# Optimization experiments

Hardware: AMD Instinct MI355X
Metric: run time of the kernel (lower is better)

## Reference

```python
import jax, jax.numpy as jnp
import numpy as np

N = 8192
E = 262144
F_IN, H1, H2 = 512, 256, 128


def setup_inputs() -> dict:
    key = jax.random.key(0)
    ks = jax.random.split(key, 7)
    x = jax.random.normal(ks[0], (N, F_IN), dtype=jnp.float32)
    # glorot-ish init scale
    W1 = jax.random.normal(ks[1], (F_IN, H1), dtype=jnp.float32) * (1.0 / np.sqrt(F_IN))
    W2 = jax.random.normal(ks[2], (H1, H2), dtype=jnp.float32) * (1.0 / np.sqrt(H1))
    W3 = jax.random.normal(ks[3], (H1, H2), dtype=jnp.float32) * (1.0 / np.sqrt(H1))
    edge_w = jax.random.uniform(ks[4], (E,), dtype=jnp.float32) / 32.0  # ~normalized adj
    row = jax.random.randint(ks[5], (E,), 0, N, dtype=jnp.int64)
    col = jax.random.randint(ks[6], (E,), 0, N, dtype=jnp.int64)
    return {"x": x, "W1": W1, "W2": W2, "W3": W3, "edge_w": edge_w, "row": row, "col": col}


def _spmm(row, col, edge_w, h):
    # sparse adjacency aggregate: out[i] = sum_{e: row[e]==i} edge_w[e] * h[col[e]]
    msgs = edge_w[:, None] * h[col]  # [E, d]
    return jax.ops.segment_sum(msgs, row, num_segments=N)


def reference(x, W1, W2, W3, edge_w, row, col):
    # gc1: dropout(off, eval) -> matmul -> spmm -> relu
    h1 = jax.nn.relu(_spmm(row, col, edge_w, x @ W1))  # [N, H1]
    # gc2 / gc3: identity activation
    mu = _spmm(row, col, edge_w, h1 @ W2)              # [N, H2]
    logvar = _spmm(row, col, edge_w, h1 @ W3)          # [N, H2]
    z = mu  # eval-mode reparameterize returns mu
    adj_rec = z @ z.T  # [N, N], decoder act = identity
    return (h1, adj_rec, mu, logvar, z)
```

## Files before the change

kernel.cpp:

```cpp
#include <hip/hip_runtime.h>

typedef __bf16 bf16_t;
typedef __bf16 bf16x4 __attribute__((ext_vector_type(4)));
typedef __bf16 bf16x8 __attribute__((ext_vector_type(8)));
typedef float floatx4 __attribute__((ext_vector_type(4)));

static constexpr int NN  = 8192;
static constexpr int FIN = 512;
static constexpr int NH1 = 256;
static constexpr int NH2 = 128;
static constexpr int NE  = 262144;
static constexpr int CAP = 128;

static constexpr size_t OFF_H1     = 0;
static constexpr size_t OFF_ADJ    = (size_t)NN * NH1;
static constexpr size_t OFF_MU     = OFF_ADJ + (size_t)NN * NN;
static constexpr size_t OFF_LOGVAR = OFF_MU + (size_t)NN * NH2;
static constexpr size_t OFF_Z      = OFF_LOGVAR + (size_t)NN * NH2;

template <int KD, int RT, bool ABF, int EPI>
__device__ __forceinline__ void gemm_body(
    int bx, int by, const float* __restrict__ Af, const bf16_t* __restrict__ Abf,
    const bf16_t* __restrict__ BT, float* __restrict__ C, int ldc,
    float* __restrict__ dout, bf16_t* __restrict__ zb, int ldz,
    float* __restrict__ L, int lane, int wid) {
  const int l15 = lane & 15;
  const int lg  = lane >> 4;
  const int brow = by * (RT * 32) + (wid >> 1) * (RT * 16);
  const int bcol = bx * 128 + (wid & 1) * 64;

  floatx4 acc[RT][4];
#pragma unroll
  for (int i = 0; i < RT; ++i)
#pragma unroll
    for (int j = 0; j < 4; ++j) acc[i][j] = (floatx4){0.f, 0.f, 0.f, 0.f};

#pragma unroll 1
  for (int kk = 0; kk < KD; kk += 32) {
    bf16x8 a[RT], b[4];
#pragma unroll
    for (int rt = 0; rt < RT; ++rt) {
      const int r = brow + rt * 16 + l15;
      if constexpr (ABF) {
        a[rt] = *(const bf16x8*)(Abf + (size_t)r * KD + kk + lg * 8);
      } else {
        const float* p = Af + (size_t)r * KD + kk + lg * 8;
        const floatx4 lo = *(const floatx4*)p;
        const floatx4 hi = *(const floatx4*)(p + 4);
        bf16x8 t;
        t[0] = (bf16_t)lo[0]; t[1] = (bf16_t)lo[1];
        t[2] = (bf16_t)lo[2]; t[3] = (bf16_t)lo[3];
        t[4] = (bf16_t)hi[0]; t[5] = (bf16_t)hi[1];
        t[6] = (bf16_t)hi[2]; t[7] = (bf16_t)hi[3];
        a[rt] = t;
      }
    }
#pragma unroll
    for (int ct = 0; ct < 4; ++ct) {
      const int c = bcol + ct * 16 + l15;
      b[ct] = *(const bf16x8*)(BT + (size_t)c * KD + kk + lg * 8);
    }
#pragma unroll
    for (int rt = 0; rt < RT; ++rt)
#pragma unroll
      for (int ct = 0; ct < 4; ++ct)
        acc[rt][ct] = __builtin_amdgcn_mfma_f32_16x16x32_bf16(
            a[rt], b[ct], acc[rt][ct], 0, 0, 0);
  }

#pragma unroll
  for (int rt = 0; rt < RT; ++rt) {
#pragma unroll
    for (int ct = 0; ct < 4; ++ct)
#pragma unroll
      for (int r = 0; r < 4; ++r)
        L[(lg * 4 + r) * 68 + ct * 16 + l15] = acc[rt][ct][r];
    __builtin_amdgcn_wave_barrier();
#pragma unroll
    for (int it = 0; it < 4; ++it) {
      const int idx = it * 64 + lane;
      const int rr = idx >> 4, c4 = idx & 15;
      const floatx4 v = *(const floatx4*)(L + rr * 68 + c4 * 4);
      const int orow = brow + rt * 16 + rr;
      const int gc = bcol + c4 * 4;
      if constexpr (EPI == 0) {
        __builtin_nontemporal_store(v, (floatx4*)(C + (size_t)orow * ldc + gc));
      } else if constexpr (EPI == 1) {
        if (gc < NH2) {
          __builtin_nontemporal_store(
              v, (floatx4*)(dout + OFF_MU + (size_t)orow * NH2 + gc));
          __builtin_nontemporal_store(
              v, (floatx4*)(dout + OFF_Z + (size_t)orow * NH2 + gc));
          bf16x4 o;
          o[0] = (bf16_t)v[0]; o[1] = (bf16_t)v[1];
          o[2] = (bf16_t)v[2]; o[3] = (bf16_t)v[3];
          *(bf16x4*)(zb + (size_t)orow * ldz + gc) = o;
        } else {
          __builtin_nontemporal_store(
              v, (floatx4*)(dout + OFF_LOGVAR + (size_t)orow * NH2 + gc - NH2));
        }
      } else {
        bf16x4 o;
        o[0] = (bf16_t)v[0]; o[1] = (bf16_t)v[1];
        o[2] = (bf16_t)v[2]; o[3] = (bf16_t)v[3];
        *(bf16x4*)(zb + (size_t)orow * ldz + gc) = o;
      }
    }
    __builtin_amdgcn_wave_barrier();
  }
}

__global__ __launch_bounds__(256) void k_prep(
    const float* __restrict__ W1, const float* __restrict__ W2,
    const float* __restrict__ W3, bf16_t* __restrict__ W1T,
    bf16_t* __restrict__ W23T, int* __restrict__ counts) {
  const int gid = blockIdx.x * 256 + threadIdx.x;
  if (gid <= NN) counts[gid] = 0;
  if (gid < NH1 * FIN) {
    const int n = gid >> 9, k = gid & 511;
    W1T[gid] = (bf16_t)W1[k * NH1 + n];
  }
  if (gid < NH1 * NH1) {
    const int n = gid >> 8, k = gid & 255;
    W23T[gid] = (bf16_t)(n < NH2 ? W2[k * NH2 + n] : W3[k * NH2 + (n - NH2)]);
  }
}

__global__ __launch_bounds__(256) void k_fat(
    const float* __restrict__ x, const bf16_t* __restrict__ W1T,
    bf16_t* __restrict__ XWb, const int* __restrict__ row,
    const int* __restrict__ col, const float* __restrict__ edge_w,
    int* __restrict__ counts, uint2* __restrict__ bucket,
    uint4* __restrict__ spill) {
  __shared__ float lt[4][16 * 68];
  const int bid = blockIdx.x;
  if (bid < 256) {
    const int lane = threadIdx.x & 63;
    const int wid  = threadIdx.x >> 6;
    gemm_body<FIN, 2, false, 2>(bid & 1, bid >> 1, x, nullptr, W1T, nullptr, 0,
                                nullptr, XWb, NH1, lt[wid], lane, wid);
  } else {
    const int e = (bid - 256) * 256 + threadIdx.x;
    const int r = row[e];
    const int p = atomicAdd(&counts[r], 1);
    if (p < CAP) {
      uint2 v;
      v.x = (unsigned)col[e];
      v.y = __float_as_uint(edge_w[e]);
      bucket[(size_t)r * CAP + p] = v;
    } else {
      const int s = atomicAdd(&counts[NN], 1);
      uint4 v;
      v.x = (unsigned)r; v.y = (unsigned)col[e];
      v.z = __float_as_uint(edge_w[e]); v.w = 0;
      spill[s] = v;
    }
  }
}

template <bool RELU>
__global__ __launch_bounds__(256) void spmm_bucket(
    const int* __restrict__ counts, const uint2* __restrict__ bucket,
    const uint4* __restrict__ spill, const bf16_t* __restrict__ src,
    float* __restrict__ dst_f, bf16_t* __restrict__ dst_b) {
  const int lane = threadIdx.x & 63;
  const int r = blockIdx.x * 4 + (threadIdx.x >> 6);
  const int li = lane & 15;
  const int g  = lane >> 4;
  const int deg = min(counts[r], CAP);
  float acc[16];
#pragma unroll
  for (int c = 0; c < 16; ++c) acc[c] = 0.f;

  for (int base = 0; base < deg; base += 64) {
    const int t = base + lane;
    uint2 cw;
    cw.x = 0; cw.y = 0;
    if (t < deg) cw = bucket[(size_t)r * CAP + t];
    const int cnt = min(64, deg - base);
#pragma unroll 2
    for (int j4 = 0; j4 < cnt; j4 += 4) {
      const int cj = __shfl((int)cw.x, j4 + g);
      const float wj = __shfl(__uint_as_float(cw.y), j4 + g);
      const bf16_t* p = src + (size_t)cj * NH1 + li * 16;
      const bf16x8 v0 = *(const bf16x8*)p;
      const bf16x8 v1 = *(const bf16x8*)(p + 8);
#pragma unroll
      for (int c = 0; c < 8; ++c) {
        acc[c]     += wj * (float)v0[c];
        acc[8 + c] += wj * (float)v1[c];
      }
    }
  }
  const int ns = counts[NN];
  if (ns > 0 && g == 0) {
    for (int i = 0; i < ns; ++i) {
      const uint4 s = spill[i];
      if ((int)s.x == r) {
        const float wj = __uint_as_float(s.z);
        const bf16_t* p = src + (size_t)s.y * NH1 + li * 16;
        const bf16x8 v0 = *(const bf16x8*)p;
        const bf16x8 v1 = *(const bf16x8*)(p + 8);
#pragma unroll
        for (int c = 0; c < 8; ++c) {
          acc[c]     += wj * (float)v0[c];
          acc[8 + c] += wj * (float)v1[c];
        }
      }
    }
  }
#pragma unroll
  for (int c = 0; c < 16; ++c) {
    acc[c] += __shfl_xor(acc[c], 16);
    acc[c] += __shfl_xor(acc[c], 32);
    if constexpr (RELU) acc[c] = fmaxf(acc[c], 0.f);
  }
  float o0, o1, o2, o3;
  switch (g) {
    case 0:  o0 = acc[0];  o1 = acc[1];  o2 = acc[2];  o3 = acc[3];  break;
    case 1:  o0 = acc[4];  o1 = acc[5];  o2 = acc[6];  o3 = acc[7];  break;
    case 2:  o0 = acc[8];  o1 = acc[9];  o2 = acc[10]; o3 = acc[11]; break;
    default: o0 = acc[12]; o1 = acc[13]; o2 = acc[14]; o3 = acc[15]; break;
  }
  const int ch = li * 16 + g * 4;
  if (dst_f) {
    floatx4 o = (floatx4){o0, o1, o2, o3};
    __builtin_nontemporal_store(o, (floatx4*)(dst_f + (size_t)r * NH1 + ch));
  }
  if (dst_b) {
    bf16x4 o;
    o[0] = (bf16_t)o0; o[1] = (bf16_t)o1; o[2] = (bf16_t)o2; o[3] = (bf16_t)o3;
    *(bf16x4*)(dst_b + (size_t)r * NH1 + ch) = o;
  }
}

template <int KD, int RT, bool ABF, int EPI, bool SWZ>
__global__ __launch_bounds__(256) void mfma_gemm(
    const float* __restrict__ Af, const bf16_t* __restrict__ Abf,
    const bf16_t* __restrict__ BT, float* __restrict__ C, int ldc,
    float* __restrict__ dout, bf16_t* __restrict__ zb, int ldz) {
  __shared__ float lt[4][16 * 68];
  int bx, by;
  if constexpr (SWZ) {
    const int bid = blockIdx.x;
    const int s = (bid & 7) * 512 + (bid >> 3);
    by = s >> 6; bx = s & 63;
  } else {
    bx = blockIdx.x; by = blockIdx.y;
  }
  const int lane = threadIdx.x & 63;
  const int wid  = threadIdx.x >> 6;
  gemm_body<KD, RT, ABF, EPI>(bx, by, Af, Abf, BT, C, ldc, dout, zb, ldz,
                              lt[wid], lane, wid);
}

extern "C" void kernel_launch(void* const* d_in, const int* in_sizes, int n_in,
                              void* d_out, int out_size, void* d_ws, size_t ws_size,
                              hipStream_t stream) {
  const float* x      = (const float*)d_in[0];
  const float* W1     = (const float*)d_in[1];
  const float* W2     = (const float*)d_in[2];
  const float* W3     = (const float*)d_in[3];
  const float* edge_w = (const float*)d_in[4];
  const int*   row    = (const int*)d_in[5];
  const int*   col    = (const int*)d_in[6];
  float* out = (float*)d_out;
  char*  ws  = (char*)d_ws;

  bf16_t* XWb  = (bf16_t*)(ws);
  bf16_t* h1b  = (bf16_t*)(ws + (4u << 20));
  bf16_t* W1T  = (bf16_t*)(ws + (8u << 20));
  bf16_t* W23T = (bf16_t*)(ws + (8u << 20) + (1u << 18));
  int*    counts = (int*)(ws + (8u << 20) + (3u << 18));
  uint2*  bucket = (uint2*)(ws + (9u << 20));
  uint4*  spill  = (uint4*)(ws + (17u << 20));
  bf16_t* gb  = XWb;
  bf16_t* zbf = h1b;

  k_prep<<<512, 256, 0, stream>>>(W1, W2, W3, W1T, W23T, counts);
  k_fat<<<1280, 256, 0, stream>>>(x, W1T, XWb, row, col, edge_w, counts, bucket,
                                  spill);
  spmm_bucket<true><<<NN / 4, 256, 0, stream>>>(counts, bucket, spill, XWb,
                                                out + OFF_H1, h1b);
  spmm_bucket<false><<<NN / 4, 256, 0, stream>>>(counts, bucket, spill, h1b,
                                                 nullptr, gb);
  mfma_gemm<NH1, 2, true, 1, false><<<dim3(2, 128), 256, 0, stream>>>(
      nullptr, gb, W23T, nullptr, 0, out, zbf, NH2);
  mfma_gemm<NH2, 4, true, 0, true><<<4096, 256, 0, stream>>>(
      nullptr, zbf, zbf, out + OFF_ADJ, NN, nullptr, nullptr, 0);
}
```

Baseline: 141.2 us.

## Fuse second SpMM with W2/W3 GEMM into one kernel per 16-row block

Replaces the separate non-ReLU SpMM and the following W23 MFMA GEMM with a single kernel. Each 1024-thread block gathers 16 rows of A·h1 into LDS as bf16, then applies a 16x16x32 MFMA against W23T to produce mu, z and logvar directly. This removes one launch and the global write and read of the intermediate aggregate. In exchange, W23T is read from global memory by every block, and the large 1024-thread blocks may reduce occupancy flexibility.

```diff
diff --git a/kernel.cpp b/kernel.cpp
--- a/kernel.cpp
+++ b/kernel.cpp
@@ -22,8 +22,7 @@
 __device__ __forceinline__ void gemm_body(
     int bx, int by, const float* __restrict__ Af, const bf16_t* __restrict__ Abf,
     const bf16_t* __restrict__ BT, float* __restrict__ C, int ldc,
-    float* __restrict__ dout, bf16_t* __restrict__ zb, int ldz,
-    float* __restrict__ L, int lane, int wid) {
+    bf16_t* __restrict__ zb, int ldz, float* __restrict__ L, int lane, int wid) {
   const int l15 = lane & 15;
   const int lg  = lane >> 4;
   const int brow = by * (RT * 32) + (wid >> 1) * (RT * 16);
@@ -85,20 +84,6 @@
       const int gc = bcol + c4 * 4;
       if constexpr (EPI == 0) {
         __builtin_nontemporal_store(v, (floatx4*)(C + (size_t)orow * ldc + gc));
-      } else if constexpr (EPI == 1) {
-        if (gc < NH2) {
-          __builtin_nontemporal_store(
-              v, (floatx4*)(dout + OFF_MU + (size_t)orow * NH2 + gc));
-          __builtin_nontemporal_store(
-              v, (floatx4*)(dout + OFF_Z + (size_t)orow * NH2 + gc));
-          bf16x4 o;
-          o[0] = (bf16_t)v[0]; o[1] = (bf16_t)v[1];
-          o[2] = (bf16_t)v[2]; o[3] = (bf16_t)v[3];
-          *(bf16x4*)(zb + (size_t)orow * ldz + gc) = o;
-        } else {
-          __builtin_nontemporal_store(
-              v, (floatx4*)(dout + OFF_LOGVAR + (size_t)orow * NH2 + gc - NH2));
-        }
       } else {
         bf16x4 o;
         o[0] = (bf16_t)v[0]; o[1] = (bf16_t)v[1];
@@ -138,7 +123,7 @@
     const int lane = threadIdx.x & 63;
     const int wid  = threadIdx.x >> 6;
     gemm_body<FIN, 2, false, 2>(bid & 1, bid >> 1, x, nullptr, W1T, nullptr, 0,
-                                nullptr, XWb, NH1, lt[wid], lane, wid);
+                                XWb, NH1, lt[wid], lane, wid);
   } else {
     const int e = (bid - 256) * 256 + threadIdx.x;
     const int r = row[e];
@@ -158,20 +143,12 @@
   }
 }
 
-template <bool RELU>
-__global__ __launch_bounds__(256) void spmm_bucket(
-    const int* __restrict__ counts, const uint2* __restrict__ bucket,
-    const uint4* __restrict__ spill, const bf16_t* __restrict__ src,
-    float* __restrict__ dst_f, bf16_t* __restrict__ dst_b) {
-  const int lane = threadIdx.x & 63;
-  const int r = blockIdx.x * 4 + (threadIdx.x >> 6);
-  const int li = lane & 15;
-  const int g  = lane >> 4;
-  const int deg = min(counts[r], CAP);
-  float acc[16];
+__device__ __forceinline__ void spmm_gather_row(
+    int r, int deg, const uint2* __restrict__ bucket,
+    const uint4* __restrict__ spill, int ns, const bf16_t* __restrict__ src,
+    int lane, int li, int g, float* __restrict__ acc) {
 #pragma unroll
   for (int c = 0; c < 16; ++c) acc[c] = 0.f;
-
   for (int base = 0; base < deg; base += 64) {
     const int t = base + lane;
     uint2 cw;
@@ -192,7 +169,6 @@
       }
     }
   }
-  const int ns = counts[NN];
   if (ns > 0 && g == 0) {
     for (int i = 0; i < ns; ++i) {
       const uint4 s = spill[i];
@@ -209,11 +185,24 @@
       }
     }
   }
+}
+
+__global__ __launch_bounds__(256) void spmm_bucket_relu(
+    const int* __restrict__ counts, const uint2* __restrict__ bucket,
+    const uint4* __restrict__ spill, const bf16_t* __restrict__ src,
+    float* __restrict__ dst_f, bf16_t* __restrict__ dst_b) {
+  const int lane = threadIdx.x & 63;
+  const int r = blockIdx.x * 4 + (threadIdx.x >> 6);
+  const int li = lane & 15;
+  const int g  = lane >> 4;
+  const int deg = min(counts[r], CAP);
+  float acc[16];
+  spmm_gather_row(r, deg, bucket, spill, counts[NN], src, lane, li, g, acc);
 #pragma unroll
   for (int c = 0; c < 16; ++c) {
     acc[c] += __shfl_xor(acc[c], 16);
     acc[c] += __shfl_xor(acc[c], 32);
-    if constexpr (RELU) acc[c] = fmaxf(acc[c], 0.f);
+    acc[c] = fmaxf(acc[c], 0.f);
   }
   float o0, o1, o2, o3;
   switch (g) {
@@ -223,14 +212,71 @@
     default: o0 = acc[12]; o1 = acc[13]; o2 = acc[14]; o3 = acc[15]; break;
   }
   const int ch = li * 16 + g * 4;
-  if (dst_f) {
-    floatx4 o = (floatx4){o0, o1, o2, o3};
-    __builtin_nontemporal_store(o, (floatx4*)(dst_f + (size_t)r * NH1 + ch));
-  }
-  if (dst_b) {
-    bf16x4 o;
-    o[0] = (bf16_t)o0; o[1] = (bf16_t)o1; o[2] = (bf16_t)o2; o[3] = (bf16_t)o3;
-    *(bf16x4*)(dst_b + (size_t)r * NH1 + ch) = o;
+  floatx4 o = (floatx4){o0, o1, o2, o3};
+  __builtin_nontemporal_store(o, (floatx4*)(dst_f + (size_t)r * NH1 + ch));
+  bf16x4 ob;
+  ob[0] = (bf16_t)o0; ob[1] = (bf16_t)o1; ob[2] = (bf16_t)o2; ob[3] = (bf16_t)o3;
+  *(bf16x4*)(dst_b + (size_t)r * NH1 + ch) = ob;
+}
+
+__global__ __launch_bounds__(1024) void k_fuse23(
+    const int* __restrict__ counts, const uint2* __restrict__ bucket,
+    const uint4* __restrict__ spill, const bf16_t* __restrict__ h1b,
+    const bf16_t* __restrict__ W23T, float* __restrict__ dout,
+    bf16_t* __restrict__ zbf) {
+  __shared__ bf16_t Lg[16][264];
+  const int lane = threadIdx.x & 63;
+  const int wid  = threadIdx.x >> 6;
+  const int li = lane & 15;
+  const int g  = lane >> 4;
+  const int l15 = li;
+  const int lg  = g;
+  const int r0 = blockIdx.x * 16;
+  const int r  = r0 + wid;
+
+  const int deg = min(counts[r], CAP);
+  float acc[16];
+  spmm_gather_row(r, deg, bucket, spill, counts[NN], h1b, lane, li, g, acc);
+#pragma unroll
+  for (int c = 0; c < 16; ++c) {
+    acc[c] += __shfl_xor(acc[c], 16);
+    acc[c] += __shfl_xor(acc[c], 32);
+  }
+  float o0, o1, o2, o3;
+  switch (g) {
+    case 0:  o0 = acc[0];  o1 = acc[1];  o2 = acc[2];  o3 = acc[3];  break;
+    case 1:  o0 = acc[4];  o1 = acc[5];  o2 = acc[6];  o3 = acc[7];  break;
+    case 2:  o0 = acc[8];  o1 = acc[9];  o2 = acc[10]; o3 = acc[11]; break;
+    default: o0 = acc[12]; o1 = acc[13]; o2 = acc[14]; o3 = acc[15]; break;
+  }
+  bf16x4 gv;
+  gv[0] = (bf16_t)o0; gv[1] = (bf16_t)o1; gv[2] = (bf16_t)o2; gv[3] = (bf16_t)o3;
+  *(bf16x4*)(&Lg[wid][li * 16 + g * 4]) = gv;
+  __syncthreads();
+
+  const int wc = wid * 16;
+  floatx4 a2 = (floatx4){0.f, 0.f, 0.f, 0.f};
+#pragma unroll
+  for (int kk = 0; kk < NH1; kk += 32) {
+    const bf16x8 af = *(const bf16x8*)(&Lg[l15][kk + lg * 8]);
+    const bf16x8 bw =
+        *(const bf16x8*)(W23T + (size_t)(wc + l15) * NH1 + kk + lg * 8);
+    a2 = __builtin_amdgcn_mfma_f32_16x16x32_bf16(bw, af, a2, 0, 0, 0);
+  }
+  const int orow = r0 + l15;
+  const int oc = wc + lg * 4;
+  if (oc < NH2) {
+    __builtin_nontemporal_store(a2,
+                                (floatx4*)(dout + OFF_MU + (size_t)orow * NH2 + oc));
+    __builtin_nontemporal_store(a2,
+                                (floatx4*)(dout + OFF_Z + (size_t)orow * NH2 + oc));
+    bf16x4 ob;
+    ob[0] = (bf16_t)a2[0]; ob[1] = (bf16_t)a2[1];
+    ob[2] = (bf16_t)a2[2]; ob[3] = (bf16_t)a2[3];
+    *(bf16x4*)(zbf + (size_t)orow * NH2 + oc) = ob;
+  } else {
+    __builtin_nontemporal_store(
+        a2, (floatx4*)(dout + OFF_LOGVAR + (size_t)orow * NH2 + oc - NH2));
   }
 }
 
@@ -238,7 +284,7 @@
 __global__ __launch_bounds__(256) void mfma_gemm(
     const float* __restrict__ Af, const bf16_t* __restrict__ Abf,
     const bf16_t* __restrict__ BT, float* __restrict__ C, int ldc,
-    float* __restrict__ dout, bf16_t* __restrict__ zb, int ldz) {
+    bf16_t* __restrict__ zb, int ldz) {
   __shared__ float lt[4][16 * 68];
   int bx, by;
   if constexpr (SWZ) {
@@ -250,8 +296,8 @@
   }
   const int lane = threadIdx.x & 63;
   const int wid  = threadIdx.x >> 6;
-  gemm_body<KD, RT, ABF, EPI>(bx, by, Af, Abf, BT, C, ldc, dout, zb, ldz,
-                              lt[wid], lane, wid);
+  gemm_body<KD, RT, ABF, EPI>(bx, by, Af, Abf, BT, C, ldc, zb, ldz, lt[wid],
+                              lane, wid);
 }
 
 extern "C" void kernel_launch(void* const* d_in, const int* in_sizes, int n_in,
@@ -274,18 +320,15 @@
   int*    counts = (int*)(ws + (8u << 20) + (3u << 18));
   uint2*  bucket = (uint2*)(ws + (9u << 20));
   uint4*  spill  = (uint4*)(ws + (17u << 20));
-  bf16_t* gb  = XWb;
-  bf16_t* zbf = h1b;
+  bf16_t* zbf  = (bf16_t*)(ws + (17u << 20) + (1u << 16));
 
   k_prep<<<512, 256, 0, stream>>>(W1, W2, W3, W1T, W23T, counts);
   k_fat<<<1280, 256, 0, stream>>>(x, W1T, XWb, row, col, edge_w, counts, bucket,
                                   spill);
-  spmm_bucket<true><<<NN / 4, 256, 0, stream>>>(counts, bucket, spill, XWb,
-                                                out + OFF_H1, h1b);
-  spmm_bucket<false><<<NN / 4, 256, 0, stream>>>(counts, bucket, spill, h1b,
-                                                 nullptr, gb);
-  mfma_gemm<NH1, 2, true, 1, false><<<dim3(2, 128), 256, 0, stream>>>(
-      nullptr, gb, W23T, nullptr, 0, out, zbf, NH2);
+  spmm_bucket_relu<<<NN / 4, 256, 0, stream>>>(counts, bucket, spill, XWb,
+                                               out + OFF_H1, h1b);
+  k_fuse23<<<NN / 16, 1024, 0, stream>>>(counts, bucket, spill, h1b, W23T, out,
+                                         zbf);
   mfma_gemm<NH2, 4, true, 0, true><<<4096, 256, 0, stream>>>(
-      nullptr, zbf, zbf, out + OFF_ADJ, NN, nullptr, nullptr, 0);
-}
+      nullptr, zbf, zbf, out + OFF_ADJ, NN, nullptr, 0);
+}
```

After: 138.9 us. No clear change (-1.6%).
